# Performance work log

Measured on AMD Instinct MI355X. Metric: run time of the kernel, lower is better.

Reference implementation:

```python
import jax, jax.numpy as jnp
import numpy as np

B, C, H, W = 32, 256, 56, 56
WS = 7            # window size (grid/dilated windows)
NH = 4            # num heads = C // dim_head
DH = 64           # dim_head
CMID = 256        # dim_mid = dim_in * exp_ratio
EPS = 1e-5


def _depthwise(x, w):
    # x: (b, C, h, w), w: (C, 1, k, k), 'same' padding, groups=C
    return jax.lax.conv_general_dilated(
        x, w, window_strides=(1, 1), padding='SAME',
        feature_group_count=x.shape[1],
        dimension_numbers=('NCHW', 'OIHW', 'NCHW'))


def setup_inputs() -> dict:
    key = jax.random.key(0)
    ks = jax.random.split(key, 12)
    return {
        'x': jax.random.normal(ks[0], (B, C, H, W), jnp.float32),
        'bn_gamma': jnp.ones((C,), jnp.float32),
        'bn_beta': jnp.zeros((C,), jnp.float32),
        'bn_mean': jnp.zeros((C,), jnp.float32),
        'bn_var': jnp.ones((C,), jnp.float32),
        'w_qk': jax.random.normal(ks[1], (2 * C, C), jnp.float32) * 0.05,
        'w_v': jax.random.normal(ks[2], (CMID, C), jnp.float32) * 0.05,
        'w_conv3': jax.random.normal(ks[3], (CMID, 1, 3, 3), jnp.float32) * 0.1,
        'w_conv5': jax.random.normal(ks[4], (CMID, 1, 5, 5), jnp.float32) * 0.1,
        'w_conv7': jax.random.normal(ks[5], (CMID, 1, 7, 7), jnp.float32) * 0.1,
        'attn_w': jax.random.uniform(ks[6], (1, CMID, 1, 1), jnp.float32),
        'c3_w': jax.random.uniform(ks[7], (1, CMID, 1, 1), jnp.float32),
        'c5_w': jax.random.uniform(ks[8], (1, CMID, 1, 1), jnp.float32),
        'c7_w': jax.random.uniform(ks[9], (1, CMID, 1, 1), jnp.float32),
        'w_proj': jax.random.normal(ks[10], (C, CMID), jnp.float32) * 0.05,
    }


def reference(x, bn_gamma, bn_beta, bn_mean, bn_var, w_qk, w_v,
              w_conv3, w_conv5, w_conv7, attn_w, c3_w, c5_w, c7_w, w_proj):
    shortcut = x
    # BatchNorm2d (eval mode, running stats)
    g = (bn_gamma / jnp.sqrt(bn_var + EPS))[None, :, None, None]
    x = (x - bn_mean[None, :, None, None]) * g + bn_beta[None, :, None, None]

    Bc, Cc, Hc, Wc = x.shape
    n1, n2 = Hc // WS, Wc // WS
    # grid/dilated windowing: 'b c (h1 n1) (w1 n2) -> (b n1 n2) c h1 w1'
    xw = (x.reshape(Bc, Cc, WS, n1, WS, n2)
           .transpose(0, 3, 5, 1, 2, 4)
           .reshape(Bc * n1 * n2, Cc, WS, WS))
    b = xw.shape[0]
    hw = WS * WS

    # qk 1x1 conv -> split into per-head q, k: (b, nh, hw, dh)
    qk = jnp.einsum('oc,bchw->bohw', w_qk, xw).reshape(b, 2, NH, DH, hw)
    q = qk[:, 0].transpose(0, 1, 3, 2)
    k = qk[:, 1].transpose(0, 1, 3, 2)

    # v 1x1 conv (attn_pre=False: attention over projected v)
    v = jnp.einsum('oc,bchw->bohw', w_v, xw)  # (b, CMID, ws, ws)
    vh = v.reshape(b, NH, CMID // NH, hw).transpose(0, 1, 3, 2)

    scale = 1.0 / jnp.sqrt(jnp.asarray(DH, x.dtype))
    attn = jax.nn.softmax(jnp.einsum('bnqd,bnkd->bnqk', q, k) * scale, axis=-1)
    x_spa = (jnp.einsum('bnqk,bnkd->bnqd', attn, vh)
             .transpose(0, 1, 3, 2).reshape(b, CMID, WS, WS))

    # multi-scale depthwise conv branch + weighted fusion + residual
    c3 = _depthwise(v, w_conv3)
    c5 = _depthwise(v, w_conv5)
    c7 = _depthwise(v, w_conv7)
    xc = x_spa * attn_w + c3 * c3_w + c5 * c5_w + c7 * c7_w + v

    # unwindow: '(b n1 n2) c h1 w1 -> b c (h1 n1) (w1 n2)'
    x = (xc.reshape(Bc, n1, n2, CMID, WS, WS)
           .transpose(0, 3, 4, 1, 5, 2)
           .reshape(Bc, CMID, Hc, Wc))

    # output 1x1 projection + residual (drop/drop_path are 0)
    x = jnp.einsum('oc,bchw->bohw', w_proj, x)
    return shortcut + x
```

## Files before the change

### kernel.cpp

```cpp
#include <hip/hip_runtime.h>
#include <cstddef>
#include <cstdint>

typedef short bf16x8 __attribute__((ext_vector_type(8)));
typedef float f32x4 __attribute__((ext_vector_type(4)));

#define MFMA16(a, b, c) __builtin_amdgcn_mfma_f32_16x16x32_bf16((a), (b), (c), 0, 0, 0)

__device__ __forceinline__ unsigned short f2bf(float f) {
  unsigned u = __float_as_uint(f);
  u = (u + 0x7FFFu + ((u >> 16) & 1u)) >> 16;
  return (unsigned short)u;
}
__device__ __forceinline__ float bf2f(unsigned short h) {
  return __uint_as_float(((unsigned)h) << 16);
}

__global__ void wprep(const float* __restrict__ bn_g, const float* __restrict__ bn_b,
                      const float* __restrict__ bn_m, const float* __restrict__ bn_v,
                      const float* __restrict__ w_qk, const float* __restrict__ w_v,
                      const float* __restrict__ w_proj,
                      const float* __restrict__ w3, const float* __restrict__ w5,
                      const float* __restrict__ w7,
                      unsigned short* __restrict__ Wqk, unsigned short* __restrict__ Wv,
                      unsigned short* __restrict__ Wp,
                      float* __restrict__ bqk, float* __restrict__ bv,
                      float* __restrict__ w3T, float* __restrict__ w5T,
                      float* __restrict__ w7T) {
  int blk = blockIdx.x, t = threadIdx.x;
  if (blk == 4) {
    for (int idx = t; idx < 21248; idx += 256) {
      if (idx < 2304) {
        int k2 = idx >> 8, c = idx & 255;
        w3T[idx] = w3[c * 9 + k2];
      } else if (idx < 8704) {
        int i = idx - 2304;
        int k2 = i >> 8, c = i & 255;
        w5T[i] = w5[c * 25 + k2];
      } else {
        int i = idx - 8704;
        int k2 = i >> 8, c = i & 255;
        w7T[i] = w7[c * 49 + k2];
      }
    }
    return;
  }
  int o = blk * 256 + t;
  if (o < 512) {
    float scale = (o < 256) ? 0.125f : 1.0f;
    float bias = 0.f;
    for (int c = 0; c < 256; ++c) {
      float g = bn_g[c] / sqrtf(bn_v[c] + 1e-5f);
      float be = bn_b[c] - bn_m[c] * g;
      float wv = w_qk[o * 256 + c];
      bias += wv * be;
      Wqk[o * 256 + c] = f2bf(wv * g * scale);
    }
    bqk[o] = bias * scale;
  } else if (o < 768) {
    int oo = o - 512;
    float bias = 0.f;
    for (int c = 0; c < 256; ++c) {
      float g = bn_g[c] / sqrtf(bn_v[c] + 1e-5f);
      float be = bn_b[c] - bn_m[c] * g;
      float wv = w_v[oo * 256 + c];
      bias += wv * be;
      Wv[oo * 256 + c] = f2bf(wv * g);
    }
    bv[oo] = bias;
  } else {
    int oo = o - 768;
    for (int c = 0; c < 256; ++c) Wp[oo * 256 + c] = f2bf(w_proj[oo * 256 + c]);
  }
}

__global__ __launch_bounds__(256) void xpose(const float* __restrict__ x,
                                             unsigned short* __restrict__ xT) {
  __shared__ float tile[64 * 68];
  int blk = blockIdx.x;
  int bb = blk / 196;
  int rem = blk - bb * 196;
  int cblk = rem / 49;
  int pblk = rem - cblk * 49;
  int t = threadIdx.x;
  {
    int r = t >> 2, seg = t & 3;
    const float* src = x + (size_t)bb * 802816 + (size_t)(cblk * 64 + r) * 3136 +
                       pblk * 64 + seg * 16;
    float4 v0 = ((const float4*)src)[0];
    float4 v1 = ((const float4*)src)[1];
    float4 v2 = ((const float4*)src)[2];
    float4 v3 = ((const float4*)src)[3];
    float* td = tile + r * 68 + seg * 16;
    td[0] = v0.x; td[1] = v0.y; td[2] = v0.z; td[3] = v0.w;
    td[4] = v1.x; td[5] = v1.y; td[6] = v1.z; td[7] = v1.w;
    td[8] = v2.x; td[9] = v2.y; td[10] = v2.z; td[11] = v2.w;
    td[12] = v3.x; td[13] = v3.y; td[14] = v3.z; td[15] = v3.w;
  }
  __syncthreads();
  {
    int p = t >> 2, cs = t & 3;
    alignas(16) unsigned short tmp[16];
#pragma unroll
    for (int u = 0; u < 16; ++u) tmp[u] = f2bf(tile[(cs * 16 + u) * 68 + p]);
    unsigned short* dst = xT + (size_t)(bb * 3136 + pblk * 64 + p) * 256 +
                          cblk * 64 + cs * 16;
    ((uint4*)dst)[0] = *(const uint4*)(tmp);
    ((uint4*)dst)[1] = *(const uint4*)(tmp + 8);
  }
}

__global__ __launch_bounds__(512, 4) void k2_win(
    const unsigned short* __restrict__ xT, const unsigned short* __restrict__ Wqk,
    const unsigned short* __restrict__ Wv, const float* __restrict__ bqk,
    const float* __restrict__ bv, const float* __restrict__ w3T,
    const float* __restrict__ w5T, const float* __restrict__ w7T,
    const float* __restrict__ aw, const float* __restrict__ c3w,
    const float* __restrict__ c5w, const float* __restrict__ c7w,
    unsigned short* __restrict__ xcT) {
  extern __shared__ char smem[];
  unsigned short* xw = (unsigned short*)smem;
  unsigned short* v_lds = (unsigned short*)(smem + 25872);
  unsigned short* q_lds = (unsigned short*)(smem + 33152);
  unsigned short* k_lds = (unsigned short*)(smem + 42368);
  unsigned short* Sb = (unsigned short*)(smem + 51584);
  float* spa = (float*)(smem + 60800);

  const int tid = threadIdx.x;
  const int l = tid & 63, w = tid >> 6, l15 = l & 15, lg = l >> 4;
  const int blk = blockIdx.x;
  const int bb = blk >> 6, i1 = (blk >> 3) & 7, i2 = blk & 7;

  for (int idx = tid; idx < 1568; idx += 512) {
    int r = idx >> 5, seg = idx & 31;
    int h1 = (r * 9363) >> 16, w1 = r - h1 * 7;
    int pix = bb * 3136 + (h1 * 8 + i1) * 56 + w1 * 8 + i2;
    *(uint4*)(xw + r * 264 + seg * 8) =
        *(const uint4*)(xT + (size_t)pix * 256 + seg * 8);
  }
  if (tid < 8) v_lds[64 * 56 + tid] = 0;
  __syncthreads();

  for (int h = 0; h < 4; ++h) {
    {
      const bool isq = (w < 4);
      const int wt = isq ? w : (w - 4);
      const int obase = isq ? (h * 64 + wt * 16) : (256 + h * 64 + wt * 16);
      f32x4 aq[4], av[4];
#pragma unroll
      for (int nt = 0; nt < 4; ++nt) {
        aq[nt] = (f32x4){0.f, 0.f, 0.f, 0.f};
        av[nt] = (f32x4){0.f, 0.f, 0.f, 0.f};
      }
#pragma unroll 2
      for (int ks = 0; ks < 8; ++ks) {
        bf16x8 b[4];
#pragma unroll
        for (int nt = 0; nt < 4; ++nt) {
          int j = nt * 16 + l15;
          if (j > 48) j = 48;
          b[nt] = *(const bf16x8*)(xw + j * 264 + ks * 32 + lg * 8);
        }
        bf16x8 a0 = *(const bf16x8*)(Wqk + (obase + l15) * 256 + ks * 32 + lg * 8);
#pragma unroll
        for (int nt = 0; nt < 4; ++nt) aq[nt] = MFMA16(a0, b[nt], aq[nt]);
        if (isq) {
          bf16x8 a1 =
              *(const bf16x8*)(Wv + (h * 64 + wt * 16 + l15) * 256 + ks * 32 + lg * 8);
#pragma unroll
          for (int nt = 0; nt < 4; ++nt) av[nt] = MFMA16(a1, b[nt], av[nt]);
        }
      }
      unsigned short* dst = isq ? q_lds : k_lds;
#pragma unroll
      for (int ri = 0; ri < 4; ++ri) {
        float bias = bqk[obase + lg * 4 + ri];
        int d = wt * 16 + lg * 4 + ri;
#pragma unroll
        for (int nt = 0; nt < 4; ++nt) {
          int p = nt * 16 + l15;
          dst[p * 72 + d] = f2bf(aq[nt][ri] + bias);
        }
      }
      if (isq) {
#pragma unroll
        for (int ri = 0; ri < 4; ++ri) {
          int cl = wt * 16 + lg * 4 + ri;
          float bvv = bv[h * 64 + cl];
#pragma unroll
          for (int nt = 0; nt < 4; ++nt) {
            int p = nt * 16 + l15;
            if (p < 56) v_lds[cl * 56 + p] = f2bf(av[nt][ri] + bvv);
          }
        }
      }
    }
    __syncthreads();

    if (w < 4) {
      f32x4 s[4];
#pragma unroll
      for (int nt = 0; nt < 4; ++nt) s[nt] = (f32x4){0.f, 0.f, 0.f, 0.f};
#pragma unroll
      for (int ks = 0; ks < 2; ++ks) {
        bf16x8 a = *(const bf16x8*)(q_lds + (w * 16 + l15) * 72 + ks * 32 + lg * 8);
        bf16x8 b[4];
#pragma unroll
        for (int nt = 0; nt < 4; ++nt)
          b[nt] = *(const bf16x8*)(k_lds + (nt * 16 + l15) * 72 + ks * 32 + lg * 8);
#pragma unroll
        for (int nt = 0; nt < 4; ++nt) s[nt] = MFMA16(a, b[nt], s[nt]);
      }
#pragma unroll
      for (int ri = 0; ri < 4; ++ri) {
        float s0 = s[0][ri], s1 = s[1][ri], s2 = s[2][ri], s3 = s[3][ri];
        if (l15 != 0) s3 = -1e30f;
        float m = fmaxf(fmaxf(s0, s1), fmaxf(s2, s3));
        m = fmaxf(m, __shfl_xor(m, 1));
        m = fmaxf(m, __shfl_xor(m, 2));
        m = fmaxf(m, __shfl_xor(m, 4));
        m = fmaxf(m, __shfl_xor(m, 8));
        float e0 = __expf(s0 - m), e1 = __expf(s1 - m);
        float e2 = __expf(s2 - m), e3 = __expf(s3 - m);
        float sum = e0 + e1 + e2 + e3;
        sum += __shfl_xor(sum, 1);
        sum += __shfl_xor(sum, 2);
        sum += __shfl_xor(sum, 4);
        sum += __shfl_xor(sum, 8);
        float inv = 1.f / sum;
        int row = w * 16 + lg * 4 + ri;
        unsigned short* sb = Sb + row * 72 + l15;
        sb[0] = f2bf(e0 * inv);
        sb[16] = f2bf(e1 * inv);
        sb[32] = f2bf(e2 * inv);
        sb[48] = f2bf(e3 * inv);
      }
    }
    __syncthreads();

    {
      int pr = w & 3, nc = (w >> 2) * 2;
      f32x4 acc[2];
      acc[0] = (f32x4){0.f, 0.f, 0.f, 0.f};
      acc[1] = (f32x4){0.f, 0.f, 0.f, 0.f};
#pragma unroll
      for (int ks = 0; ks < 2; ++ks) {
        bf16x8 a = *(const bf16x8*)(Sb + (pr * 16 + l15) * 72 + ks * 32 + lg * 8);
#pragma unroll
        for (int t = 0; t < 2; ++t) {
          bf16x8 b = *(const bf16x8*)(v_lds + ((nc + t) * 16 + l15) * 56 +
                                      ks * 32 + lg * 8);
          acc[t] = MFMA16(a, b, acc[t]);
        }
      }
#pragma unroll
      for (int t = 0; t < 2; ++t) {
        int cl = (nc + t) * 16 + l15;
#pragma unroll
        for (int ri = 0; ri < 4; ++ri) {
          int p = pr * 16 + lg * 4 + ri;
          if (p < 49) spa[cl * 52 + p] = acc[t][ri];
        }
      }
    }
    __syncthreads();

    if (w < 7) {
      int cl = l;
      int c = h * 64 + cl;
      int hr = w;
      float awc = aw[c], c3c = c3w[c], c5c = c5w[c], c7c = c7w[c];
      float s3a[7], s5a[7], s7a[7], vcen[7];
#pragma unroll
      for (int ww = 0; ww < 7; ++ww) {
        s3a[ww] = 0.f; s5a[ww] = 0.f; s7a[ww] = 0.f;
      }
#pragma unroll 1
      for (int dyi = 0; dyi < 7; ++dyi) {
        int ry = hr + dyi - 3;
        if ((unsigned)ry < 7u) {
          float vrow[7];
#pragma unroll
          for (int cc = 0; cc < 7; ++cc)
            vrow[cc] = bf2f(v_lds[cl * 56 + ry * 7 + cc]);
          if (dyi == 3) {
#pragma unroll
            for (int cc = 0; cc < 7; ++cc) vcen[cc] = vrow[cc];
          }
#pragma unroll
          for (int dx = 0; dx < 7; ++dx) {
            float wv = w7T[(dyi * 7 + dx) * 256 + c];
#pragma unroll
            for (int ww = 0; ww < 7; ++ww) {
              int cc = ww + dx - 3;
              if (cc >= 0 && cc < 7) s7a[ww] = fmaf(wv, vrow[cc], s7a[ww]);
            }
          }
          if (dyi >= 1 && dyi <= 5) {
#pragma unroll
            for (int dx = 0; dx < 5; ++dx) {
              float wv = w5T[((dyi - 1) * 5 + dx) * 256 + c];
#pragma unroll
              for (int ww = 0; ww < 7; ++ww) {
                int cc = ww + dx - 2;
                if (cc >= 0 && cc < 7) s5a[ww] = fmaf(wv, vrow[cc], s5a[ww]);
              }
            }
          }
          if (dyi >= 2 && dyi <= 4) {
#pragma unroll
            for (int dx = 0; dx < 3; ++dx) {
              float wv = w3T[((dyi - 2) * 3 + dx) * 256 + c];
#pragma unroll
              for (int ww = 0; ww < 7; ++ww) {
                int cc = ww + dx - 1;
                if (cc >= 0 && cc < 7) s3a[ww] = fmaf(wv, vrow[cc], s3a[ww]);
              }
            }
          }
        }
      }
      float sp[7];
#pragma unroll
      for (int ww = 0; ww < 7; ++ww) sp[ww] = spa[cl * 52 + hr * 7 + ww];
#pragma unroll
      for (int ww = 0; ww < 7; ++ww) {
        float val = fmaf(sp[ww], awc,
                    fmaf(s3a[ww], c3c,
                    fmaf(s5a[ww], c5c,
                    fmaf(s7a[ww], c7c, vcen[ww]))));
        int pixp = bb * 3136 + (hr * 8 + i1) * 56 + ww * 8 + i2;
        xcT[(size_t)pixp * 256 + c] = f2bf(val);
      }
    }
    __syncthreads();
  }
}

__global__ __launch_bounds__(256) void k3_proj(const unsigned short* __restrict__ Wp,
                                               const unsigned short* __restrict__ xcT,
                                               const float* __restrict__ x,
                                               float* __restrict__ out) {
  const int tid = threadIdx.x, l = tid & 63, w = tid >> 6;
  const int l15 = l & 15, lg = l >> 4;
  const int blk = blockIdx.x;
  f32x4 acc[4][4];
#pragma unroll
  for (int mf = 0; mf < 4; ++mf)
#pragma unroll
    for (int nf = 0; nf < 4; ++nf) acc[mf][nf] = (f32x4){0.f, 0.f, 0.f, 0.f};
#pragma unroll 2
  for (int ks = 0; ks < 8; ++ks) {
    bf16x8 a[4], b[4];
#pragma unroll
    for (int mf = 0; mf < 4; ++mf)
      a[mf] = *(const bf16x8*)(Wp + (w * 64 + mf * 16 + l15) * 256 + ks * 32 + lg * 8);
#pragma unroll
    for (int nf = 0; nf < 4; ++nf)
      b[nf] = *(const bf16x8*)(xcT + (size_t)(blk * 64 + nf * 16 + l15) * 256 +
                               ks * 32 + lg * 8);
#pragma unroll
    for (int mf = 0; mf < 4; ++mf)
#pragma unroll
      for (int nf = 0; nf < 4; ++nf) acc[mf][nf] = MFMA16(a[mf], b[nf], acc[mf][nf]);
  }
  int bb = (blk * 64) / 3136;
  int loc0 = blk * 64 - bb * 3136;
#pragma unroll
  for (int mf = 0; mf < 4; ++mf)
#pragma unroll
    for (int nf = 0; nf < 4; ++nf)
#pragma unroll
      for (int ri = 0; ri < 4; ++ri) {
        int o = w * 64 + mf * 16 + lg * 4 + ri;
        int ploc = loc0 + nf * 16 + l15;
        size_t addr = (size_t)bb * 802816 + (size_t)o * 3136 + ploc;
        out[addr] = x[addr] + acc[mf][nf][ri];
      }
}

extern "C" void kernel_launch(void* const* d_in, const int* in_sizes, int n_in,
                              void* d_out, int out_size, void* d_ws, size_t ws_size,
                              hipStream_t stream) {
  const float* x = (const float*)d_in[0];
  const float* bn_g = (const float*)d_in[1];
  const float* bn_b = (const float*)d_in[2];
  const float* bn_m = (const float*)d_in[3];
  const float* bn_v = (const float*)d_in[4];
  const float* w_qk = (const float*)d_in[5];
  const float* w_v = (const float*)d_in[6];
  const float* w3 = (const float*)d_in[7];
  const float* w5 = (const float*)d_in[8];
  const float* w7 = (const float*)d_in[9];
  const float* aw = (const float*)d_in[10];
  const float* c3w = (const float*)d_in[11];
  const float* c5w = (const float*)d_in[12];
  const float* c7w = (const float*)d_in[13];
  const float* w_pr = (const float*)d_in[14];
  float* out = (float*)d_out;
  char* ws = (char*)d_ws;

  unsigned short* Wqk = (unsigned short*)ws;
  unsigned short* Wv = (unsigned short*)(ws + 262144);
  unsigned short* Wp = (unsigned short*)(ws + 393216);
  float* bqk = (float*)(ws + 524288);
  float* bv = (float*)(ws + 526336);
  float* w3T = (float*)(ws + 527360);
  float* w5T = (float*)(ws + 536576);
  float* w7T = (float*)(ws + 562176);
  unsigned short* xT = (unsigned short*)(ws + 1048576);
  unsigned short* xcT = (unsigned short*)(ws + 52428800);

  wprep<<<5, 256, 0, stream>>>(bn_g, bn_b, bn_m, bn_v, w_qk, w_v, w_pr, w3, w5, w7,
                               Wqk, Wv, Wp, bqk, bv, w3T, w5T, w7T);
  xpose<<<6272, 256, 0, stream>>>(x, xT);
  hipFuncSetAttribute(reinterpret_cast<const void*>(k2_win),
                      hipFuncAttributeMaxDynamicSharedMemorySize, 74112);
  k2_win<<<2048, 512, 74112, stream>>>(xT, Wqk, Wv, bqk, bv, w3T, w5T, w7T, aw, c3w,
                                       c5w, c7w, xcT);
  k3_proj<<<1568, 256, 0, stream>>>(Wp, xcT, x, out);
}
```

Before: 352.3 us.

## Software-pipeline next head's QKV projections behind softmax and PV in k2_win

Head 0's Q/K/V projection moves into a prologue. Inside the head loop, waves 4-7 compute the next head's V projection while waves 0-3 run QK^T and softmax. They then compute the next head's Q/K while waves 0-3 do the PV product. V is double-buffered in LDS, which removes one barrier per head and puts previously idle waves to work. The cost is more LDS per block (81392 bytes), uneven work across waves, and only half the waves doing the PV matmul.

New measurement: 346.2 us. No clear change (-1.7%).

```diff
diff --git a/kernel.cpp b/kernel.cpp
--- a/kernel.cpp
+++ b/kernel.cpp
@@ -120,11 +120,12 @@
     unsigned short* __restrict__ xcT) {
   extern __shared__ char smem[];
   unsigned short* xw = (unsigned short*)smem;
-  unsigned short* v_lds = (unsigned short*)(smem + 25872);
-  unsigned short* q_lds = (unsigned short*)(smem + 33152);
-  unsigned short* k_lds = (unsigned short*)(smem + 42368);
-  unsigned short* Sb = (unsigned short*)(smem + 51584);
-  float* spa = (float*)(smem + 60800);
+  unsigned short* vbuf0 = (unsigned short*)(smem + 25872);
+  unsigned short* vbuf1 = (unsigned short*)(smem + 33152);
+  unsigned short* q_lds = (unsigned short*)(smem + 40432);
+  unsigned short* k_lds = (unsigned short*)(smem + 49648);
+  unsigned short* Sb = (unsigned short*)(smem + 58864);
+  float* spa = (float*)(smem + 68080);
 
   const int tid = threadIdx.x;
   const int l = tid & 63, w = tid >> 6, l15 = l & 15, lg = l >> 4;
@@ -138,64 +139,67 @@
     *(uint4*)(xw + r * 264 + seg * 8) =
         *(const uint4*)(xT + (size_t)pix * 256 + seg * 8);
   }
-  if (tid < 8) v_lds[64 * 56 + tid] = 0;
+  if (tid < 8) vbuf0[64 * 56 + tid] = 0;
+  else if (tid < 16) vbuf1[64 * 56 + (tid - 8)] = 0;
   __syncthreads();
 
+  {
+    const bool isq = (w < 4);
+    const int wt = isq ? w : (w - 4);
+    const int obase = isq ? (wt * 16) : (256 + wt * 16);
+    f32x4 aq[4], av[4];
+#pragma unroll
+    for (int nt = 0; nt < 4; ++nt) {
+      aq[nt] = (f32x4){0.f, 0.f, 0.f, 0.f};
+      av[nt] = (f32x4){0.f, 0.f, 0.f, 0.f};
+    }
+#pragma unroll 2
+    for (int ks = 0; ks < 8; ++ks) {
+      bf16x8 b[4];
+#pragma unroll
+      for (int nt = 0; nt < 4; ++nt) {
+        int j = nt * 16 + l15;
+        if (j > 48) j = 48;
+        b[nt] = *(const bf16x8*)(xw + j * 264 + ks * 32 + lg * 8);
+      }
+      bf16x8 a0 = *(const bf16x8*)(Wqk + (obase + l15) * 256 + ks * 32 + lg * 8);
+#pragma unroll
+      for (int nt = 0; nt < 4; ++nt) aq[nt] = MFMA16(a0, b[nt], aq[nt]);
+      if (isq) {
+        bf16x8 a1 = *(const bf16x8*)(Wv + (wt * 16 + l15) * 256 + ks * 32 + lg * 8);
+#pragma unroll
+        for (int nt = 0; nt < 4; ++nt) av[nt] = MFMA16(a1, b[nt], av[nt]);
+      }
+    }
+    unsigned short* dst = isq ? q_lds : k_lds;
+#pragma unroll
+    for (int ri = 0; ri < 4; ++ri) {
+      float bias = bqk[obase + lg * 4 + ri];
+      int d = wt * 16 + lg * 4 + ri;
+#pragma unroll
+      for (int nt = 0; nt < 4; ++nt) {
+        int p = nt * 16 + l15;
+        dst[p * 72 + d] = f2bf(aq[nt][ri] + bias);
+      }
+    }
+    if (isq) {
+#pragma unroll
+      for (int ri = 0; ri < 4; ++ri) {
+        int cl = wt * 16 + lg * 4 + ri;
+        float bvv = bv[cl];
+#pragma unroll
+        for (int nt = 0; nt < 4; ++nt) {
+          int p = nt * 16 + l15;
+          if (p < 56) vbuf0[cl * 56 + p] = f2bf(av[nt][ri] + bvv);
+        }
+      }
+    }
+  }
+  __syncthreads();
+
   for (int h = 0; h < 4; ++h) {
-    {
-      const bool isq = (w < 4);
-      const int wt = isq ? w : (w - 4);
-      const int obase = isq ? (h * 64 + wt * 16) : (256 + h * 64 + wt * 16);
-      f32x4 aq[4], av[4];
-#pragma unroll
-      for (int nt = 0; nt < 4; ++nt) {
-        aq[nt] = (f32x4){0.f, 0.f, 0.f, 0.f};
-        av[nt] = (f32x4){0.f, 0.f, 0.f, 0.f};
-      }
-#pragma unroll 2
-      for (int ks = 0; ks < 8; ++ks) {
-        bf16x8 b[4];
-#pragma unroll
-        for (int nt = 0; nt < 4; ++nt) {
-          int j = nt * 16 + l15;
-          if (j > 48) j = 48;
-          b[nt] = *(const bf16x8*)(xw + j * 264 + ks * 32 + lg * 8);
-        }
-        bf16x8 a0 = *(const bf16x8*)(Wqk + (obase + l15) * 256 + ks * 32 + lg * 8);
-#pragma unroll
-        for (int nt = 0; nt < 4; ++nt) aq[nt] = MFMA16(a0, b[nt], aq[nt]);
-        if (isq) {
-          bf16x8 a1 =
-              *(const bf16x8*)(Wv + (h * 64 + wt * 16 + l15) * 256 + ks * 32 + lg * 8);
-#pragma unroll
-          for (int nt = 0; nt < 4; ++nt) av[nt] = MFMA16(a1, b[nt], av[nt]);
-        }
-      }
-      unsigned short* dst = isq ? q_lds : k_lds;
-#pragma unroll
-      for (int ri = 0; ri < 4; ++ri) {
-        float bias = bqk[obase + lg * 4 + ri];
-        int d = wt * 16 + lg * 4 + ri;
-#pragma unroll
-        for (int nt = 0; nt < 4; ++nt) {
-          int p = nt * 16 + l15;
-          dst[p * 72 + d] = f2bf(aq[nt][ri] + bias);
-        }
-      }
-      if (isq) {
-#pragma unroll
-        for (int ri = 0; ri < 4; ++ri) {
-          int cl = wt * 16 + lg * 4 + ri;
-          float bvv = bv[h * 64 + cl];
-#pragma unroll
-          for (int nt = 0; nt < 4; ++nt) {
-            int p = nt * 16 + l15;
-            if (p < 56) v_lds[cl * 56 + p] = f2bf(av[nt][ri] + bvv);
-          }
-        }
-      }
-    }
-    __syncthreads();
+    unsigned short* vcur = (h & 1) ? vbuf1 : vbuf0;
+    unsigned short* vnxt = (h & 1) ? vbuf0 : vbuf1;
 
     if (w < 4) {
       f32x4 s[4];
@@ -235,31 +239,98 @@
         sb[32] = f2bf(e2 * inv);
         sb[48] = f2bf(e3 * inv);
       }
+    } else if (h < 3) {
+      int wt = w - 4;
+      f32x4 av[4];
+#pragma unroll
+      for (int nt = 0; nt < 4; ++nt) av[nt] = (f32x4){0.f, 0.f, 0.f, 0.f};
+#pragma unroll 2
+      for (int ks = 0; ks < 8; ++ks) {
+        bf16x8 b[4];
+#pragma unroll
+        for (int nt = 0; nt < 4; ++nt) {
+          int j = nt * 16 + l15;
+          if (j > 48) j = 48;
+          b[nt] = *(const bf16x8*)(xw + j * 264 + ks * 32 + lg * 8);
+        }
+        bf16x8 a1 = *(const bf16x8*)(Wv + ((h + 1) * 64 + wt * 16 + l15) * 256 +
+                                     ks * 32 + lg * 8);
+#pragma unroll
+        for (int nt = 0; nt < 4; ++nt) av[nt] = MFMA16(a1, b[nt], av[nt]);
+      }
+#pragma unroll
+      for (int ri = 0; ri < 4; ++ri) {
+        int cl = wt * 16 + lg * 4 + ri;
+        float bvv = bv[(h + 1) * 64 + cl];
+#pragma unroll
+        for (int nt = 0; nt < 4; ++nt) {
+          int p = nt * 16 + l15;
+          if (p < 56) vnxt[cl * 56 + p] = f2bf(av[nt][ri] + bvv);
+        }
+      }
     }
     __syncthreads();
 
-    {
-      int pr = w & 3, nc = (w >> 2) * 2;
-      f32x4 acc[2];
-      acc[0] = (f32x4){0.f, 0.f, 0.f, 0.f};
-      acc[1] = (f32x4){0.f, 0.f, 0.f, 0.f};
+    if (w < 4) {
+      int pr = w;
+      f32x4 acc[4];
+#pragma unroll
+      for (int t = 0; t < 4; ++t) acc[t] = (f32x4){0.f, 0.f, 0.f, 0.f};
 #pragma unroll
       for (int ks = 0; ks < 2; ++ks) {
         bf16x8 a = *(const bf16x8*)(Sb + (pr * 16 + l15) * 72 + ks * 32 + lg * 8);
 #pragma unroll
-        for (int t = 0; t < 2; ++t) {
-          bf16x8 b = *(const bf16x8*)(v_lds + ((nc + t) * 16 + l15) * 56 +
-                                      ks * 32 + lg * 8);
+        for (int t = 0; t < 4; ++t) {
+          bf16x8 b = *(const bf16x8*)(vcur + (t * 16 + l15) * 56 + ks * 32 + lg * 8);
           acc[t] = MFMA16(a, b, acc[t]);
         }
       }
 #pragma unroll
-      for (int t = 0; t < 2; ++t) {
-        int cl = (nc + t) * 16 + l15;
+      for (int t = 0; t < 4; ++t) {
+        int cl = t * 16 + l15;
 #pragma unroll
         for (int ri = 0; ri < 4; ++ri) {
           int p = pr * 16 + lg * 4 + ri;
           if (p < 49) spa[cl * 52 + p] = acc[t][ri];
+        }
+      }
+    } else if (h < 3) {
+      int wt = w - 4;
+      int obq = (h + 1) * 64 + wt * 16;
+      int obk = 256 + (h + 1) * 64 + wt * 16;
+      f32x4 aq[4], ak[4];
+#pragma unroll
+      for (int nt = 0; nt < 4; ++nt) {
+        aq[nt] = (f32x4){0.f, 0.f, 0.f, 0.f};
+        ak[nt] = (f32x4){0.f, 0.f, 0.f, 0.f};
+      }
+#pragma unroll 2
+      for (int ks = 0; ks < 8; ++ks) {
+        bf16x8 b[4];
+#pragma unroll
+        for (int nt = 0; nt < 4; ++nt) {
+          int j = nt * 16 + l15;
+          if (j > 48) j = 48;
+          b[nt] = *(const bf16x8*)(xw + j * 264 + ks * 32 + lg * 8);
+        }
+        bf16x8 a0 = *(const bf16x8*)(Wqk + (obq + l15) * 256 + ks * 32 + lg * 8);
+        bf16x8 a1 = *(const bf16x8*)(Wqk + (obk + l15) * 256 + ks * 32 + lg * 8);
+#pragma unroll
+        for (int nt = 0; nt < 4; ++nt) {
+          aq[nt] = MFMA16(a0, b[nt], aq[nt]);
+          ak[nt] = MFMA16(a1, b[nt], ak[nt]);
+        }
+      }
+#pragma unroll
+      for (int ri = 0; ri < 4; ++ri) {
+        float biasq = bqk[obq + lg * 4 + ri];
+        float biask = bqk[obk + lg * 4 + ri];
+        int d = wt * 16 + lg * 4 + ri;
+#pragma unroll
+        for (int nt = 0; nt < 4; ++nt) {
+          int p = nt * 16 + l15;
+          q_lds[p * 72 + d] = f2bf(aq[nt][ri] + biasq);
+          k_lds[p * 72 + d] = f2bf(ak[nt][ri] + biask);
         }
       }
     }
@@ -282,7 +353,7 @@
           float vrow[7];
 #pragma unroll
           for (int cc = 0; cc < 7; ++cc)
-            vrow[cc] = bf2f(v_lds[cl * 56 + ry * 7 + cc]);
+            vrow[cc] = bf2f(vcur[cl * 56 + ry * 7 + cc]);
           if (dyi == 3) {
 #pragma unroll
             for (int cc = 0; cc < 7; ++cc) vcen[cc] = vrow[cc];
@@ -415,8 +486,8 @@
                                Wqk, Wv, Wp, bqk, bv, w3T, w5T, w7T);
   xpose<<<6272, 256, 0, stream>>>(x, xT);
   hipFuncSetAttribute(reinterpret_cast<const void*>(k2_win),
-                      hipFuncAttributeMaxDynamicSharedMemorySize, 74112);
-  k2_win<<<2048, 512, 74112, stream>>>(xT, Wqk, Wv, bqk, bv, w3T, w5T, w7T, aw, c3w,
+                      hipFuncAttributeMaxDynamicSharedMemorySize, 81392);
+  k2_win<<<2048, 512, 81392, stream>>>(xT, Wqk, Wv, bqk, bv, w3T, w5T, w7T, aw, c3w,
                                        c5w, c7w, xcT);
   k3_proj<<<1568, 256, 0, stream>>>(Wp, xcT, x, out);
 }
```

## Alias window-kernel LDS buffers for occupancy and read bf16 residual in projection

Applied to the files above, without the earlier changes.

The window kernel reuses the q buffer for the softmax probabilities and the k buffer for the spatial-attention output. This cuts dynamic LDS from about 74 KB to about 52 KB so more blocks fit per CU, and the launch-bounds occupancy hint goes from 4 to 6. To fit the smaller buffer, the attn@V and depthwise-conv fusion stage now runs in two 32-channel halves, adding a barrier pair and leaving half the lanes idle in the conv pass. Separately, the projection kernel stages the bf16 transposed input through LDS and uses it as the residual instead of reading fp32 x. That halves residual read traffic but lowers the shortcut's precision to bf16.

After: 513.7 us. 1.46x slower.

```diff
diff --git a/kernel.cpp b/kernel.cpp
--- a/kernel.cpp
+++ b/kernel.cpp
@@ -110,7 +110,7 @@
   }
 }
 
-__global__ __launch_bounds__(512, 4) void k2_win(
+__global__ __launch_bounds__(512, 6) void k2_win(
     const unsigned short* __restrict__ xT, const unsigned short* __restrict__ Wqk,
     const unsigned short* __restrict__ Wv, const float* __restrict__ bqk,
     const float* __restrict__ bv, const float* __restrict__ w3T,
@@ -121,15 +121,14 @@
   extern __shared__ char smem[];
   unsigned short* xw = (unsigned short*)smem;
   unsigned short* v_lds = (unsigned short*)(smem + 25872);
-  unsigned short* q_lds = (unsigned short*)(smem + 33152);
-  unsigned short* k_lds = (unsigned short*)(smem + 42368);
-  unsigned short* Sb = (unsigned short*)(smem + 51584);
-  float* spa = (float*)(smem + 60800);
+  unsigned short* qsb = (unsigned short*)(smem + 33152);
+  unsigned short* ksp = (unsigned short*)(smem + 42368);
+  float* spa32 = (float*)(smem + 42368);
 
   const int tid = threadIdx.x;
   const int l = tid & 63, w = tid >> 6, l15 = l & 15, lg = l >> 4;
-  const int blk = blockIdx.x;
-  const int bb = blk >> 6, i1 = (blk >> 3) & 7, i2 = blk & 7;
+  const int win = blockIdx.x;
+  const int bb = win >> 6, i1 = (win >> 3) & 7, i2 = win & 7;
 
   for (int idx = tid; idx < 1568; idx += 512) {
     int r = idx >> 5, seg = idx & 31;
@@ -171,7 +170,7 @@
           for (int nt = 0; nt < 4; ++nt) av[nt] = MFMA16(a1, b[nt], av[nt]);
         }
       }
-      unsigned short* dst = isq ? q_lds : k_lds;
+      unsigned short* dst = isq ? qsb : ksp;
 #pragma unroll
       for (int ri = 0; ri < 4; ++ri) {
         float bias = bqk[obase + lg * 4 + ri];
@@ -203,11 +202,11 @@
       for (int nt = 0; nt < 4; ++nt) s[nt] = (f32x4){0.f, 0.f, 0.f, 0.f};
 #pragma unroll
       for (int ks = 0; ks < 2; ++ks) {
-        bf16x8 a = *(const bf16x8*)(q_lds + (w * 16 + l15) * 72 + ks * 32 + lg * 8);
+        bf16x8 a = *(const bf16x8*)(qsb + (w * 16 + l15) * 72 + ks * 32 + lg * 8);
         bf16x8 b[4];
 #pragma unroll
         for (int nt = 0; nt < 4; ++nt)
-          b[nt] = *(const bf16x8*)(k_lds + (nt * 16 + l15) * 72 + ks * 32 + lg * 8);
+          b[nt] = *(const bf16x8*)(ksp + (nt * 16 + l15) * 72 + ks * 32 + lg * 8);
 #pragma unroll
         for (int nt = 0; nt < 4; ++nt) s[nt] = MFMA16(a, b[nt], s[nt]);
       }
@@ -229,7 +228,7 @@
         sum += __shfl_xor(sum, 8);
         float inv = 1.f / sum;
         int row = w * 16 + lg * 4 + ri;
-        unsigned short* sb = Sb + row * 72 + l15;
+        unsigned short* sb = qsb + row * 72 + l15;
         sb[0] = f2bf(e0 * inv);
         sb[16] = f2bf(e1 * inv);
         sb[32] = f2bf(e2 * inv);
@@ -238,112 +237,116 @@
     }
     __syncthreads();
 
-    {
-      int pr = w & 3, nc = (w >> 2) * 2;
-      f32x4 acc[2];
-      acc[0] = (f32x4){0.f, 0.f, 0.f, 0.f};
-      acc[1] = (f32x4){0.f, 0.f, 0.f, 0.f};
-#pragma unroll
-      for (int ks = 0; ks < 2; ++ks) {
-        bf16x8 a = *(const bf16x8*)(Sb + (pr * 16 + l15) * 72 + ks * 32 + lg * 8);
-#pragma unroll
-        for (int t = 0; t < 2; ++t) {
-          bf16x8 b = *(const bf16x8*)(v_lds + ((nc + t) * 16 + l15) * 56 +
+    for (int half = 0; half < 2; ++half) {
+      {
+        int pr = w & 3;
+        int t = half * 2 + (w >> 2);
+        f32x4 acc = (f32x4){0.f, 0.f, 0.f, 0.f};
+#pragma unroll
+        for (int ks = 0; ks < 2; ++ks) {
+          bf16x8 a = *(const bf16x8*)(qsb + (pr * 16 + l15) * 72 + ks * 32 + lg * 8);
+          bf16x8 b = *(const bf16x8*)(v_lds + (h * 64 % 64 + t * 16 + l15) * 56 +
                                       ks * 32 + lg * 8);
-          acc[t] = MFMA16(a, b, acc[t]);
-        }
-      }
-#pragma unroll
-      for (int t = 0; t < 2; ++t) {
-        int cl = (nc + t) * 16 + l15;
+          acc = MFMA16(a, b, acc);
+        }
+        int clh = (w >> 2) * 16 + l15;
 #pragma unroll
         for (int ri = 0; ri < 4; ++ri) {
           int p = pr * 16 + lg * 4 + ri;
-          if (p < 49) spa[cl * 52 + p] = acc[t][ri];
-        }
-      }
-    }
-    __syncthreads();
-
-    if (w < 7) {
-      int cl = l;
-      int c = h * 64 + cl;
-      int hr = w;
-      float awc = aw[c], c3c = c3w[c], c5c = c5w[c], c7c = c7w[c];
-      float s3a[7], s5a[7], s7a[7], vcen[7];
-#pragma unroll
-      for (int ww = 0; ww < 7; ++ww) {
-        s3a[ww] = 0.f; s5a[ww] = 0.f; s7a[ww] = 0.f;
-      }
+          if (p < 49) spa32[clh * 52 + p] = acc[ri];
+        }
+      }
+      __syncthreads();
+
+      if (w < 7 && l < 32) {
+        int clh = half * 32 + l;
+        int c = h * 64 + clh;
+        int hr = w;
+        float awc = aw[c], c3c = c3w[c], c5c = c5w[c], c7c = c7w[c];
+        float s3a[7], s5a[7], s7a[7], vcen[7];
+#pragma unroll
+        for (int ww = 0; ww < 7; ++ww) {
+          s3a[ww] = 0.f; s5a[ww] = 0.f; s7a[ww] = 0.f;
+        }
 #pragma unroll 1
-      for (int dyi = 0; dyi < 7; ++dyi) {
-        int ry = hr + dyi - 3;
-        if ((unsigned)ry < 7u) {
-          float vrow[7];
-#pragma unroll
-          for (int cc = 0; cc < 7; ++cc)
-            vrow[cc] = bf2f(v_lds[cl * 56 + ry * 7 + cc]);
-          if (dyi == 3) {
-#pragma unroll
-            for (int cc = 0; cc < 7; ++cc) vcen[cc] = vrow[cc];
-          }
-#pragma unroll
-          for (int dx = 0; dx < 7; ++dx) {
-            float wv = w7T[(dyi * 7 + dx) * 256 + c];
-#pragma unroll
-            for (int ww = 0; ww < 7; ++ww) {
-              int cc = ww + dx - 3;
-              if (cc >= 0 && cc < 7) s7a[ww] = fmaf(wv, vrow[cc], s7a[ww]);
+        for (int dyi = 0; dyi < 7; ++dyi) {
+          int ry = hr + dyi - 3;
+          if ((unsigned)ry < 7u) {
+            float vrow[7];
+#pragma unroll
+            for (int cc = 0; cc < 7; ++cc)
+              vrow[cc] = bf2f(v_lds[clh * 56 + ry * 7 + cc]);
+            if (dyi == 3) {
+#pragma unroll
+              for (int cc = 0; cc < 7; ++cc) vcen[cc] = vrow[cc];
             }
-          }
-          if (dyi >= 1 && dyi <= 5) {
-#pragma unroll
-            for (int dx = 0; dx < 5; ++dx) {
-              float wv = w5T[((dyi - 1) * 5 + dx) * 256 + c];
+#pragma unroll
+            for (int dx = 0; dx < 7; ++dx) {
+              float wv = w7T[(dyi * 7 + dx) * 256 + c];
 #pragma unroll
               for (int ww = 0; ww < 7; ++ww) {
-                int cc = ww + dx - 2;
-                if (cc >= 0 && cc < 7) s5a[ww] = fmaf(wv, vrow[cc], s5a[ww]);
+                int cc = ww + dx - 3;
+                if (cc >= 0 && cc < 7) s7a[ww] = fmaf(wv, vrow[cc], s7a[ww]);
+              }
+            }
+            if (dyi >= 1 && dyi <= 5) {
+#pragma unroll
+              for (int dx = 0; dx < 5; ++dx) {
+                float wv = w5T[((dyi - 1) * 5 + dx) * 256 + c];
+#pragma unroll
+                for (int ww = 0; ww < 7; ++ww) {
+                  int cc = ww + dx - 2;
+                  if (cc >= 0 && cc < 7) s5a[ww] = fmaf(wv, vrow[cc], s5a[ww]);
+                }
+              }
+            }
+            if (dyi >= 2 && dyi <= 4) {
+#pragma unroll
+              for (int dx = 0; dx < 3; ++dx) {
+                float wv = w3T[((dyi - 2) * 3 + dx) * 256 + c];
+#pragma unroll
+                for (int ww = 0; ww < 7; ++ww) {
+                  int cc = ww + dx - 1;
+                  if (cc >= 0 && cc < 7) s3a[ww] = fmaf(wv, vrow[cc], s3a[ww]);
+                }
               }
             }
           }
-          if (dyi >= 2 && dyi <= 4) {
-#pragma unroll
-            for (int dx = 0; dx < 3; ++dx) {
-              float wv = w3T[((dyi - 2) * 3 + dx) * 256 + c];
-#pragma unroll
-              for (int ww = 0; ww < 7; ++ww) {
-                int cc = ww + dx - 1;
-                if (cc >= 0 && cc < 7) s3a[ww] = fmaf(wv, vrow[cc], s3a[ww]);
-              }
-            }
-          }
-        }
-      }
-      float sp[7];
-#pragma unroll
-      for (int ww = 0; ww < 7; ++ww) sp[ww] = spa[cl * 52 + hr * 7 + ww];
-#pragma unroll
-      for (int ww = 0; ww < 7; ++ww) {
-        float val = fmaf(sp[ww], awc,
-                    fmaf(s3a[ww], c3c,
-                    fmaf(s5a[ww], c5c,
-                    fmaf(s7a[ww], c7c, vcen[ww]))));
-        int pixp = bb * 3136 + (hr * 8 + i1) * 56 + ww * 8 + i2;
-        xcT[(size_t)pixp * 256 + c] = f2bf(val);
-      }
-    }
-    __syncthreads();
+        }
+        float sp[7];
+#pragma unroll
+        for (int ww = 0; ww < 7; ++ww) sp[ww] = spa32[l * 52 + hr * 7 + ww];
+#pragma unroll
+        for (int ww = 0; ww < 7; ++ww) {
+          float val = fmaf(sp[ww], awc,
+                      fmaf(s3a[ww], c3c,
+                      fmaf(s5a[ww], c5c,
+                      fmaf(s7a[ww], c7c, vcen[ww]))));
+          int pixp = bb * 3136 + (hr * 8 + i1) * 56 + ww * 8 + i2;
+          xcT[(size_t)pixp * 256 + c] = f2bf(val);
+        }
+      }
+      __syncthreads();
+    }
   }
 }
 
 __global__ __launch_bounds__(256) void k3_proj(const unsigned short* __restrict__ Wp,
                                                const unsigned short* __restrict__ xcT,
-                                               const float* __restrict__ x,
+                                               const unsigned short* __restrict__ xT,
                                                float* __restrict__ out) {
+  __shared__ unsigned short xres[64 * 264];
   const int tid = threadIdx.x, l = tid & 63, w = tid >> 6;
   const int l15 = l & 15, lg = l >> 4;
   const int blk = blockIdx.x;
+
+  for (int idx = tid; idx < 2048; idx += 256) {
+    int p = idx >> 5, seg = idx & 31;
+    *(uint4*)(xres + p * 264 + seg * 8) =
+        *(const uint4*)(xT + (size_t)(blk * 64 + p) * 256 + seg * 8);
+  }
+  __syncthreads();
+
   f32x4 acc[4][4];
 #pragma unroll
   for (int mf = 0; mf < 4; ++mf)
@@ -373,9 +376,9 @@
 #pragma unroll
       for (int ri = 0; ri < 4; ++ri) {
         int o = w * 64 + mf * 16 + lg * 4 + ri;
-        int ploc = loc0 + nf * 16 + l15;
-        size_t addr = (size_t)bb * 802816 + (size_t)o * 3136 + ploc;
-        out[addr] = x[addr] + acc[mf][nf][ri];
+        int pl = nf * 16 + l15;
+        size_t addr = (size_t)bb * 802816 + (size_t)o * 3136 + loc0 + pl;
+        out[addr] = bf2f(xres[pl * 264 + o]) + acc[mf][nf][ri];
       }
 }
 
@@ -415,8 +418,8 @@
                                Wqk, Wv, Wp, bqk, bv, w3T, w5T, w7T);
   xpose<<<6272, 256, 0, stream>>>(x, xT);
   hipFuncSetAttribute(reinterpret_cast<const void*>(k2_win),
-                      hipFuncAttributeMaxDynamicSharedMemorySize, 74112);
-  k2_win<<<2048, 512, 74112, stream>>>(xT, Wqk, Wv, bqk, bv, w3T, w5T, w7T, aw, c3w,
+                      hipFuncAttributeMaxDynamicSharedMemorySize, 51584);
+  k2_win<<<2048, 512, 51584, stream>>>(xT, Wqk, Wv, bqk, bv, w3T, w5T, w7T, aw, c3w,
                                        c5w, c7w, xcT);
-  k3_proj<<<1568, 256, 0, stream>>>(Wp, xcT, x, out);
-}
+  k3_proj<<<1568, 256, 0, stream>>>(Wp, xcT, xT, out);
+}
```
